# Performance work log

Hardware: AMD Instinct MI355X
Metric: run time of the kernel (lower is better)

The kernel has to match this reference:

```python
import jax, jax.numpy as jnp
import numpy as np

B = 8192          # tokens
D = 768           # activation_dim
N_EXP = 16        # experts
ED = 1536         # expert_dict_size = dict_size // experts
DICT = N_EXP * ED # 24576
K = 100           # sparse dict top-k
TOP_E = 2         # top-e expert selection


def setup_inputs() -> dict:
    key = jax.random.key(0)
    ks = jax.random.split(key, 5)
    x = jax.random.normal(ks[0], (B, D), dtype=jnp.float32)
    gate_W = jax.random.normal(ks[1], (N_EXP, D), dtype=jnp.float32) * 0.02
    gate_b = jnp.zeros((N_EXP,), jnp.float32)
    b_gate = jnp.zeros((D,), jnp.float32)
    b_dec = jnp.zeros((D,), jnp.float32)
    expert_W = jax.random.normal(ks[2], (N_EXP, ED, D), dtype=jnp.float32) * 0.02
    expert_b = jnp.zeros((N_EXP, ED), jnp.float32)
    dec = jax.random.normal(ks[3], (DICT, D), dtype=jnp.float32)
    decoder = dec / (jnp.linalg.norm(dec, axis=1, keepdims=True) + 1.1920929e-07)  # unit-norm rows
    return {"x": x, "gate_W": gate_W, "gate_b": gate_b, "b_gate": b_gate,
            "b_dec": b_dec, "expert_W": expert_W, "expert_b": expert_b,
            "decoder": decoder}


def reference(x, gate_W, gate_b, b_gate, b_dec, expert_W, expert_b, decoder):
    nb = x.shape[0]
    # --- gate: softmax over experts, keep top-e, renormalize (heaviside=False path)
    gate_logits = (x - b_gate) @ gate_W.T + gate_b            # [B, E]
    gate_scores = jax.nn.softmax(gate_logits, axis=-1)
    top_vals, top_idx = jax.lax.top_k(gate_scores, TOP_E)     # [B, e]
    # softmax over {-inf everywhere except top values} == softmax(top_vals) scattered
    renorm = jax.nn.softmax(top_vals, axis=-1)
    expert_mask = jnp.zeros_like(gate_scores).at[
        jnp.arange(nb)[:, None], top_idx].set(renorm)          # [B, E]
    # --- dense all-expert encode (faithful to source: computes every expert, then masks)
    z = jax.nn.relu(jnp.einsum('bd,ned->bne', x - b_dec, expert_W) + expert_b)  # [B, E, ED]
    f = (z * expert_mask[:, :, None]).reshape(nb, DICT)       # [B, dict_size]
    # --- top-k sparse dict decode (TritonDecoder equivalent)
    top_acts, top_indices = jax.lax.top_k(f, K)               # [B, k]
    x_hat = jnp.einsum('bk,bkd->bd', top_acts, decoder[top_indices]) + b_dec
    return x_hat
```

## Files before the change

kernel.cpp:

```cpp
#include <hip/hip_runtime.h>
#include <hip/hip_fp16.h>
#include <cstdint>
#include <cstddef>

#define NB    8192
#define DD    768
#define NE    16
#define NPAIR 256
#define EDD   1536
#define KTOP  100
#define MAXT  8192
#define CAND_MAX 256
#define K1BLK 2048
#define NSTEP 12
#define BKBYTES 128
#define CONF_ULP 6
#define BAND_ULP 5

typedef __attribute__((ext_vector_type(4))) float f32x4;
typedef __attribute__((ext_vector_type(8))) _Float16 f16x8;

#define VMCNT8() asm volatile("s_waitcnt vmcnt(8)" ::: "memory")
#define VMCNT4() asm volatile("s_waitcnt vmcnt(4)" ::: "memory")
#define VMCNT0() asm volatile("s_waitcnt vmcnt(0)" ::: "memory")

__device__ __forceinline__ unsigned short f2bf(float v) {
    unsigned int u = __float_as_uint(v);
    u += 0x7FFFu + ((u >> 16) & 1u);
    return (unsigned short)(u >> 16);
}
__device__ __forceinline__ float bf2f(unsigned short h) {
    return __uint_as_float(((unsigned int)h) << 16);
}
__device__ __forceinline__ unsigned short f2h_bits(float v) {
    return __half_as_ushort(__float2half(v));
}
__device__ __forceinline__ float h2f_bits(unsigned short b) {
    return __half2float(__ushort_as_half(b));
}
__device__ __forceinline__ void async16(const void* g, void* l) {
    __builtin_amdgcn_global_load_lds(
        (const __attribute__((address_space(1))) unsigned int*)g,
        (__attribute__((address_space(3))) unsigned int*)l, 16, 0, 0);
}

__global__ __launch_bounds__(256) void k0_cvt_bf(
    const float* __restrict__ src, unsigned short* __restrict__ dst)
{
    const int i = blockIdx.x * 256 + threadIdx.x;
    const float4 v = reinterpret_cast<const float4*>(src)[i];
    ushort4 h;
    h.x = f2bf(v.x); h.y = f2bf(v.y); h.z = f2bf(v.z); h.w = f2bf(v.w);
    reinterpret_cast<ushort4*>(dst)[i] = h;
}

__global__ __launch_bounds__(256) void k0_cvt_f16(
    const float* __restrict__ src, unsigned short* __restrict__ dst)
{
    const int i = blockIdx.x * 256 + threadIdx.x;
    const float4 v = reinterpret_cast<const float4*>(src)[i];
    ushort4 h;
    h.x = f2h_bits(v.x); h.y = f2h_bits(v.y); h.z = f2h_bits(v.z); h.w = f2h_bits(v.w);
    reinterpret_cast<ushort4*>(dst)[i] = h;
}

__global__ __launch_bounds__(256) void k1_gate(
    const float* __restrict__ x, const float* __restrict__ gate_W,
    const float* __restrict__ gate_b, const float* __restrict__ b_gate,
    const float* __restrict__ b_dec, unsigned short* __restrict__ xf16,
    int* __restrict__ eids, double* __restrict__ entw,
    int* __restrict__ rnk, int* __restrict__ blk_cnt,
    int* __restrict__ rnk0, unsigned char* __restrict__ blk_cntp)
{
    __shared__ int cnt[NE];
    __shared__ int cntp[NPAIR];
    const int wid  = threadIdx.x >> 6;
    const int lane = threadIdx.x & 63;
    const int blk  = blockIdx.x;
    const int tok  = blk * 4 + wid;

    if (threadIdx.x < NE) cnt[threadIdx.x] = 0;
    cntp[threadIdx.x] = 0;
    __syncthreads();

    double xv[12];
#pragma unroll
    for (int j = 0; j < 12; ++j) {
        const int k = j * 64 + lane;
        const float xr = x[(size_t)tok * DD + k];
        xv[j] = (double)xr - (double)b_gate[k];
        xf16[(size_t)tok * DD + k] = f2h_bits(xr - b_dec[k]);
    }

    double myLogit = -1.0e300;
    for (int e = 0; e < NE; ++e) {
        double d = 0.0;
#pragma unroll
        for (int j = 0; j < 12; ++j)
            d += xv[j] * (double)gate_W[e * DD + j * 64 + lane];
#pragma unroll
        for (int off = 32; off > 0; off >>= 1)
            d += __shfl_xor(d, off);
        if (lane == e) myLogit = d + (double)gate_b[e];
    }

    double m = myLogit;
#pragma unroll
    for (int off = 8; off > 0; off >>= 1) {
        double o = __shfl_xor(m, off); m = (o > m) ? o : m;
    }
    double p = exp(myLogit - m);
    double ssum = p;
#pragma unroll
    for (int off = 8; off > 0; off >>= 1) ssum += __shfl_xor(ssum, off);
    const double score = p / ssum;

    const bool lt16 = (lane < NE);
    double m1 = score;
#pragma unroll
    for (int off = 8; off > 0; off >>= 1) {
        double o = __shfl_xor(m1, off); m1 = (o > m1) ? o : m1;
    }
    unsigned long long b0 = __ballot(lt16 && (score == m1));
    const int i0 = __ffsll(b0) - 1;
    double sc2 = (lane == i0) ? -1.0 : score;
    double m2 = sc2;
#pragma unroll
    for (int off = 8; off > 0; off >>= 1) {
        double o = __shfl_xor(m2, off); m2 = (o > m2) ? o : m2;
    }
    unsigned long long b1 = __ballot(lt16 && (sc2 == m2));
    const int i1 = __ffsll(b1) - 1;

    if (lane == 0) {
        const double w0 = 1.0 / (1.0 + exp(m2 - m1));
        const double w1 = 1.0 - w0;
        eids[tok * 2 + 0] = i0;
        eids[tok * 2 + 1] = i1;
        entw[tok * 2 + 0] = w0;
        entw[tok * 2 + 1] = w1;
        rnk[tok * 2 + 0] = atomicAdd(&cnt[i0], 1);
        rnk[tok * 2 + 1] = atomicAdd(&cnt[i1], 1);
        rnk0[tok] = atomicAdd(&cntp[(i0 << 4) | i1], 1);
    }
    __syncthreads();
    if (threadIdx.x < NE)
        blk_cnt[threadIdx.x * K1BLK + blk] = cnt[threadIdx.x];
    blk_cntp[(size_t)threadIdx.x * K1BLK + blk] = (unsigned char)cntp[threadIdx.x];
}

__global__ __launch_bounds__(256) void k1_scan(
    const int* __restrict__ bc, int* __restrict__ bo, int* __restrict__ counts)
{
    __shared__ int tsum[256];
    const int e = blockIdx.x;
    const int t = threadIdx.x;
    int loc[8]; int s = 0;
#pragma unroll
    for (int i = 0; i < 8; ++i) { loc[i] = s; s += bc[e * K1BLK + t * 8 + i]; }
    tsum[t] = s;
    __syncthreads();
    for (int off = 1; off < 256; off <<= 1) {
        const int u = (t >= off) ? tsum[t - off] : 0;
        __syncthreads();
        tsum[t] += u;
        __syncthreads();
    }
    const int excl = tsum[t] - s;
#pragma unroll
    for (int i = 0; i < 8; ++i) bo[e * K1BLK + t * 8 + i] = excl + loc[i];
    if (t == 255) counts[e] = tsum[255];
}

__global__ __launch_bounds__(256) void k1_scanp(
    const unsigned char* __restrict__ bcp, unsigned short* __restrict__ bop,
    int* __restrict__ countsp)
{
    __shared__ int tsum[256];
    const int pp = blockIdx.x;
    const int t = threadIdx.x;
    int loc[8]; int s = 0;
#pragma unroll
    for (int i = 0; i < 8; ++i) { loc[i] = s; s += (int)bcp[(size_t)pp * K1BLK + t * 8 + i]; }
    tsum[t] = s;
    __syncthreads();
    for (int off = 1; off < 256; off <<= 1) {
        const int u = (t >= off) ? tsum[t - off] : 0;
        __syncthreads();
        tsum[t] += u;
        __syncthreads();
    }
    const int excl = tsum[t] - s;
#pragma unroll
    for (int i = 0; i < 8; ++i)
        bop[(size_t)pp * K1BLK + t * 8 + i] = (unsigned short)(excl + loc[i]);
    if (t == 255) countsp[pp] = tsum[255];
}

__global__ __launch_bounds__(256) void k1_base(
    const int* __restrict__ countsp, int* __restrict__ basep)
{
    __shared__ int ts[256];
    const int t = threadIdx.x;
    const int v = countsp[t];
    ts[t] = v;
    __syncthreads();
    for (int off = 1; off < 256; off <<= 1) {
        const int u = (t >= off) ? ts[t - off] : 0;
        __syncthreads();
        ts[t] += u;
        __syncthreads();
    }
    basep[t] = ts[t] - v;
}

__global__ __launch_bounds__(256) void k1_scatter(
    const int* __restrict__ eids, const int* __restrict__ rnk,
    const int* __restrict__ blk_off, int* __restrict__ lists,
    const int* __restrict__ rnk0, const unsigned short* __restrict__ bop,
    const int* __restrict__ basep, int* __restrict__ tokord)
{
    const int i = blockIdx.x * 256 + threadIdx.x;
    const int e = eids[i];
    const int blk = i >> 3;
    lists[e * MAXT + blk_off[e * K1BLK + blk] + rnk[i]] = i;
    if (!(i & 1)) {
        const int tok = i >> 1;
        const int pr = (e << 4) | eids[i | 1];
        tokord[basep[pr] + (int)bop[(size_t)pr * K1BLK + blk] + rnk0[tok]] = tok;
    }
}

template<bool WBF>
__global__ __launch_bounds__(256, 2) void k2_encode(
    const unsigned short* __restrict__ xf16,
    const unsigned short* __restrict__ wf16,
    const float* __restrict__ expert_W,
    const float* __restrict__ expert_b,
    const int* __restrict__ counts, const int* __restrict__ lists,
    const double* __restrict__ entw, unsigned short* __restrict__ fbuf)
{
    const int wg  = blockIdx.x;
    const int gw  = (wg & 7) * 1536 + (wg >> 3);
    const int e   = gw / 768;
    const int rem = gw % 768;
    const int cnt = counts[e];
    const int mbase = (rem / 12) * 128;
    if (mbase >= cnt) return;
    const int rows = min(128, cnt - mbase);
    const int nbase = (rem % 12) * 128;

    __shared__ char smem[65536];

    const int t = threadIdx.x;
    const int lane = t & 63;
    const int wid = t >> 6;
    const int wm = wid >> 1, wn = wid & 1;
    const int l15 = lane & 15, q = lane >> 4;
    const int rl = lane >> 3;
    const int cg = lane & 7;
    const int xorc = (cg ^ rl) << 4;

    size_t asrc[4];
#pragma unroll
    for (int j = 0; j < 4; ++j) {
        const int r = (wid * 4 + j) * 8 + rl;
        const int rr = (r < rows) ? r : 0;
        const int tok = lists[e * MAXT + mbase + rr] >> 1;
        asrc[j] = (size_t)tok * (DD * 2) + xorc;
    }
    size_t bsrc[4];
#pragma unroll
    for (int j = 0; j < 4; ++j) {
        const int r = (wid * 4 + j) * 8 + rl;
        bsrc[j] = ((size_t)(e * EDD + nbase + r)) * (DD * 2) + xorc;
    }
    const int kq = t & 15, rg = t >> 4;

    f32x4 acc[4][4];
#pragma unroll
    for (int a = 0; a < 4; ++a)
#pragma unroll
        for (int b = 0; b < 4; ++b)
            acc[a][b] = f32x4{0.f, 0.f, 0.f, 0.f};

    auto stageA = [&](int s, char* buf) {
#pragma unroll
        for (int j = 0; j < 4; ++j)
            async16((const char*)xf16 + asrc[j] + (size_t)s * BKBYTES,
                    buf + ((wid * 4 + j) << 10));
    };
    auto stageB_async = [&](int s, char* buf) {
#pragma unroll
        for (int j = 0; j < 4; ++j)
            async16((const char*)wf16 + bsrc[j] + (size_t)s * BKBYTES,
                    buf + 16384 + ((wid * 4 + j) << 10));
    };
    auto stageB_cvt = [&](int s, char* buf) {
#pragma unroll
        for (int j = 0; j < 8; ++j) {
            const int r = rg * 8 + j;
            const float4 bv = *reinterpret_cast<const float4*>(
                expert_W + ((size_t)e * EDD + nbase + r) * DD + s * 64 + kq * 4);
            ushort4 b4;
            b4.x = f2h_bits(bv.x); b4.y = f2h_bits(bv.y);
            b4.z = f2h_bits(bv.z); b4.w = f2h_bits(bv.w);
            *reinterpret_cast<ushort4*>(
                buf + 16384 + ((r * 128 + kq * 8) ^ ((r & 7) << 4))) = b4;
        }
    };
    auto compute = [&](char* buf) {
#pragma unroll
        for (int ks = 0; ks < 2; ++ks) {
            f16x8 ah[4], bh[4];
#pragma unroll
            for (int fm = 0; fm < 4; ++fm) {
                const int row = wm * 64 + fm * 16 + l15;
                ah[fm] = *reinterpret_cast<const f16x8*>(
                    buf + row * 128 + ((ks * 64 + q * 16) ^ ((row & 7) << 4)));
            }
#pragma unroll
            for (int fn = 0; fn < 4; ++fn) {
                const int row = wn * 64 + fn * 16 + l15;
                bh[fn] = *reinterpret_cast<const f16x8*>(
                    buf + 16384 + row * 128 + ((ks * 64 + q * 16) ^ ((row & 7) << 4)));
            }
#pragma unroll
            for (int fm = 0; fm < 4; ++fm)
#pragma unroll
                for (int fn = 0; fn < 4; ++fn)
                    acc[fm][fn] = __builtin_amdgcn_mfma_f32_16x16x32_f16(
                        ah[fm], bh[fn], acc[fm][fn], 0, 0, 0);
        }
    };

    if constexpr (WBF) {
        stageA(0, smem);
        stageB_async(0, smem);
    } else {
        stageB_cvt(0, smem);
        stageA(0, smem);
    }

    for (int s = 0; s < NSTEP; ++s) {
        char* cur = smem + ((s & 1) << 15);
        char* nxt = smem + (((s & 1) ^ 1) << 15);
        if (s + 1 < NSTEP) {
            if constexpr (WBF) {
                stageA(s + 1, nxt);
                stageB_async(s + 1, nxt);
                VMCNT8();
            } else {
                stageB_cvt(s + 1, nxt);
                stageA(s + 1, nxt);
                VMCNT4();
            }
        } else {
            VMCNT0();
        }
        __syncthreads();
        compute(cur);
        __syncthreads();
    }

#pragma unroll
    for (int fm = 0; fm < 4; ++fm) {
#pragma unroll
        for (int r = 0; r < 4; ++r) {
            const int ml = wm * 64 + fm * 16 + q * 4 + r;
            if (ml >= rows) continue;
            const int ent = lists[e * MAXT + mbase + ml];
            const float ren = (float)entw[ent];
            unsigned short* fout = fbuf + (size_t)ent * EDD + nbase;
#pragma unroll
            for (int fn = 0; fn < 4; ++fn) {
                const int nl = wn * 64 + fn * 16 + l15;
                float v = acc[fm][fn][r] + expert_b[e * EDD + nbase + nl];
                v = fmaxf(v, 0.f) * ren;
                fout[nl] = f2h_bits(v);
            }
        }
    }
}

template<int DEC16>
__global__ __launch_bounds__(256) void k3_topk_decode(
    const float* __restrict__ x, const float* __restrict__ b_dec,
    const float* __restrict__ expert_W, const float* __restrict__ expert_b,
    const int* __restrict__ eids, const double* __restrict__ entw,
    const unsigned short* __restrict__ fbuf,
    const float* __restrict__ decoder, const unsigned short* __restrict__ dec16,
    const int* __restrict__ tokord, float* __restrict__ out)
{
    const int bid = blockIdx.x;
    const int tok = tokord[(bid & 7) * (NB / 8) + (bid >> 3)];
    const int t = threadIdx.x;

    __shared__ __align__(16) char arena[12288];
    unsigned short* fv   = (unsigned short*)arena;
    unsigned int*   hist = (unsigned int*)(arena + 6144);
    int*            cidx = (int*)(arena + 7168);
    double*         cval = (double*)(arena + 8192);
    float*          red  = (float*)arena;
    __shared__ unsigned int sc[256];
    __shared__ int hb_s, T_s, rem_s, tz_s, nsel_s, ncand_s, total_s, need_s;
    __shared__ int   sel_didx[KTOP];
    __shared__ float sel_act[KTOP];

    const unsigned int* frow = reinterpret_cast<const unsigned int*>(fbuf + (size_t)tok * 2 * EDD);
#pragma unroll
    for (int i = 0; i < 6; ++i)
        reinterpret_cast<unsigned int*>(fv)[t + 256 * i] = frow[t + 256 * i];
    if (t == 0) { tz_s = 0; nsel_s = 0; ncand_s = 0; }
    hist[t] = 0u;
    __syncthreads();

#pragma unroll
    for (int i = 0; i < 12; ++i) {
        const unsigned int u = fv[t + 256 * i];
        if (u) atomicAdd(&hist[u >> 8], 1u);
    }
    __syncthreads();
    sc[t] = hist[t];
    __syncthreads();
    for (int off = 1; off < 256; off <<= 1) {
        const unsigned int v2 = (t < 256 - off) ? sc[t + off] : 0u;
        __syncthreads();
        sc[t] += v2;
        __syncthreads();
    }
    {
        const unsigned int above = (t == 255) ? 0u : sc[t + 1];
        if (sc[t] >= KTOP && above < KTOP) { hb_s = t; rem_s = KTOP - (int)above; }
        if (t == 0 && sc[0] < KTOP) tz_s = 1;
    }
    __syncthreads();

    if (!tz_s) {
        hist[t] = 0u;
        __syncthreads();
        const unsigned int hb = (unsigned int)hb_s;
#pragma unroll
        for (int i = 0; i < 12; ++i) {
            const unsigned int u = fv[t + 256 * i];
            if (u && (u >> 8) == hb) atomicAdd(&hist[u & 255u], 1u);
        }
        __syncthreads();
        sc[t] = hist[t];
        __syncthreads();
        for (int off = 1; off < 256; off <<= 1) {
            const unsigned int v2 = (t < 256 - off) ? sc[t + off] : 0u;
            __syncthreads();
            sc[t] += v2;
            __syncthreads();
        }
        {
            const unsigned int rem = (unsigned int)rem_s;
            const unsigned int above = (t == 255) ? 0u : sc[t + 1];
            if (sc[t] >= rem && above < rem) T_s = (hb_s << 8) | t;
        }
        __syncthreads();
    }

    if (tz_s) {
#pragma unroll
        for (int i = 0; i < 12; ++i) {
            const int j = t + 256 * i;
            const unsigned int u = fv[j];
            if (u) {
                const int p = atomicAdd(&nsel_s, 1);
                const int slot = (j >= EDD) ? 1 : 0;
                const int n = j - slot * EDD;
                sel_didx[p] = eids[tok * 2 + slot] * EDD + n;
                sel_act[p] = h2f_bits((unsigned short)u);
            }
        }
        __syncthreads();
        if (t == 0) total_s = nsel_s;
        __syncthreads();
    } else {
        const int T = T_s;
#pragma unroll
        for (int i = 0; i < 12; ++i) {
            const int j = t + 256 * i;
            const unsigned int u = fv[j];
            if ((int)u >= T + CONF_ULP) {
                const int p = atomicAdd(&nsel_s, 1);
                const int slot = (j >= EDD) ? 1 : 0;
                const int n = j - slot * EDD;
                sel_didx[p] = eids[tok * 2 + slot] * EDD + n;
                sel_act[p] = h2f_bits((unsigned short)u);
            } else if (u != 0u && (int)u + BAND_ULP >= T) {
                const int c = atomicAdd(&ncand_s, 1);
                if (c < CAND_MAX) cidx[c] = j;
            }
        }
        __syncthreads();

        {
            const int ncand = min(ncand_s, CAND_MAX);
            const int wv = t >> 6, lane = t & 63;
            for (int c = wv; c < ncand; c += 4) {
                const int j = cidx[c];
                const int slot = (j >= EDD) ? 1 : 0;
                const int n = j - slot * EDD;
                const int ee = eids[tok * 2 + slot];
                const float* wr = expert_W + ((size_t)ee * EDD + n) * DD;
                const float* xr = x + (size_t)tok * DD;
                double d = 0.0;
#pragma unroll
                for (int jj = 0; jj < 12; ++jj) {
                    const int k = jj * 64 + lane;
                    d += ((double)xr[k] - (double)b_dec[k]) * (double)wr[k];
                }
#pragma unroll
                for (int off = 32; off > 0; off >>= 1) d += __shfl_xor(d, off);
                if (lane == 0) {
                    double z = d + (double)expert_b[ee * EDD + n];
                    if (z < 0.0) z = 0.0;
                    cval[c] = z * entw[tok * 2 + slot];
                }
            }
        }
        __syncthreads();
        if (t == 0) {
            const int ncand = min(ncand_s, CAND_MAX);
            int need = KTOP - nsel_s;
            if (need > ncand) need = ncand;
            if (need < 0) need = 0;
            need_s = need;
            total_s = nsel_s + need;
        }
        __syncthreads();

        {
            const int ncand = min(ncand_s, CAND_MAX);
            if (t < ncand) {
                const int j = cidx[t];
                const int slot = (j >= EDD) ? 1 : 0;
                const int my_didx = eids[tok * 2 + slot] * EDD + (j - slot * EDD);
                const double v = cval[t];
                int rank = 0;
                for (int i = 0; i < ncand; ++i) {
                    const int ji = cidx[i];
                    const int si = (ji >= EDD) ? 1 : 0;
                    const int di = eids[tok * 2 + si] * EDD + (ji - si * EDD);
                    const double vi = cval[i];
                    rank += (vi > v) || (vi == v && di < my_didx);
                }
                if (rank < need_s) {
                    sel_didx[nsel_s + rank] = my_didx;
                    sel_act[nsel_s + rank] = (float)v;
                }
            }
        }
        __syncthreads();
    }

    const int total = total_s;
    const int wv = t >> 6;
    const int lane = t & 63;
    float accd[12];
#pragma unroll
    for (int i = 0; i < 12; ++i) accd[i] = 0.f;

    if (DEC16) {
        auto ldrow = [&](int k, float& a, ushort4& u0, ushort4& u1, ushort4& u2) {
            a = sel_act[k];
            const char* dr = (const char*)(dec16 + (size_t)sel_didx[k] * DD) + lane * 24;
            u0 = *reinterpret_cast<const ushort4*>(dr);
            u1 = *reinterpret_cast<const ushort4*>(dr + 8);
            u2 = *reinterpret_cast<const ushort4*>(dr + 16);
        };
        auto fmarow = [&](float a, ushort4 u0, ushort4 u1, ushort4 u2) {
            accd[0] += a * bf2f(u0.x);  accd[1]  += a * bf2f(u0.y);
            accd[2] += a * bf2f(u0.z);  accd[3]  += a * bf2f(u0.w);
            accd[4] += a * bf2f(u1.x);  accd[5]  += a * bf2f(u1.y);
            accd[6] += a * bf2f(u1.z);  accd[7]  += a * bf2f(u1.w);
            accd[8] += a * bf2f(u2.x);  accd[9]  += a * bf2f(u2.y);
            accd[10] += a * bf2f(u2.z); accd[11] += a * bf2f(u2.w);
        };
        int k = wv;
        for (; k + 12 < total; k += 16) {
            float a0, a1, a2, a3;
            ushort4 p00, p01, p02, p10, p11, p12, p20, p21, p22, p30, p31, p32;
            ldrow(k,      a0, p00, p01, p02);
            ldrow(k + 4,  a1, p10, p11, p12);
            ldrow(k + 8,  a2, p20, p21, p22);
            ldrow(k + 12, a3, p30, p31, p32);
            fmarow(a0, p00, p01, p02);
            fmarow(a1, p10, p11, p12);
            fmarow(a2, p20, p21, p22);
            fmarow(a3, p30, p31, p32);
        }
        for (; k < total; k += 4) {
            float a; ushort4 q0, q1, q2;
            ldrow(k, a, q0, q1, q2);
            fmarow(a, q0, q1, q2);
        }
    } else {
        auto body = [&](int k) {
            const float a = sel_act[k];
            const float* dr = decoder + (size_t)sel_didx[k] * DD + lane * 12;
            const float4 f0 = *reinterpret_cast<const float4*>(dr);
            const float4 f1 = *reinterpret_cast<const float4*>(dr + 4);
            const float4 f2 = *reinterpret_cast<const float4*>(dr + 8);
            accd[0] += a * f0.x;  accd[1]  += a * f0.y;
            accd[2] += a * f0.z;  accd[3]  += a * f0.w;
            accd[4] += a * f1.x;  accd[5]  += a * f1.y;
            accd[6] += a * f1.z;  accd[7]  += a * f1.w;
            accd[8] += a * f2.x;  accd[9]  += a * f2.y;
            accd[10] += a * f2.z; accd[11] += a * f2.w;
        };
        int k = wv;
        for (; k + 4 < total; k += 8) { body(k); body(k + 4); }
        if (k < total) body(k);
    }

#pragma unroll
    for (int i = 0; i < 12; ++i)
        red[wv * DD + lane * 12 + i] = accd[i];
    __syncthreads();
#pragma unroll
    for (int i = 0; i < 3; ++i) {
        const int j = t + 256 * i;
        out[(size_t)tok * DD + j] =
            red[j] + red[DD + j] + red[2 * DD + j] + red[3 * DD + j] + b_dec[j];
    }
}

__global__ void k_sentinel(float* __restrict__ out, int n) {
    int i = blockIdx.x * blockDim.x + threadIdx.x;
    if (i < n) out[i] = 12345.0f;
}

extern "C" void kernel_launch(void* const* d_in, const int* in_sizes, int n_in,
                              void* d_out, int out_size, void* d_ws, size_t ws_size,
                              hipStream_t stream)
{
    (void)in_sizes; (void)n_in;
    const float* x        = (const float*)d_in[0];
    const float* gate_W   = (const float*)d_in[1];
    const float* gate_b   = (const float*)d_in[2];
    const float* b_gate   = (const float*)d_in[3];
    const float* b_dec    = (const float*)d_in[4];
    const float* expert_W = (const float*)d_in[5];
    const float* expert_b = (const float*)d_in[6];
    const float* decoder  = (const float*)d_in[7];
    float* out = (float*)d_out;

    char* ws = (char*)d_ws;
    const size_t off_countsp = 1024;
    const size_t off_basep  = 2048;
    const size_t off_blkcnt = 4096;
    const size_t off_blkoff = off_blkcnt + (size_t)NE * K1BLK * 4;
    const size_t off_rnk    = off_blkoff + (size_t)NE * K1BLK * 4;
    const size_t off_eids   = off_rnk    + (size_t)NB * 2 * 4;
    const size_t off_entw   = off_eids   + (size_t)NB * 2 * 4;
    const size_t off_lists  = off_entw   + (size_t)NB * 2 * 8;
    const size_t off_fbuf   = off_lists  + (size_t)NE * MAXT * 4;
    const size_t off_xbf    = off_fbuf   + (size_t)NB * 2 * EDD * 2;
    const size_t off_bcp    = off_xbf    + (size_t)NB * DD * 2;
    const size_t off_bop    = off_bcp    + (size_t)NPAIR * K1BLK;
    const size_t off_rnk0   = off_bop    + (size_t)NPAIR * K1BLK * 2;
    const size_t off_tokord = off_rnk0   + (size_t)NB * 4;
    const size_t base_end   = off_tokord + (size_t)NB * 4;
    const size_t WSZ        = (size_t)NE * EDD * DD * 2;

    if (ws_size < base_end) {
        k_sentinel<<<(out_size + 255) / 256, 256, 0, stream>>>(out, out_size);
        return;
    }
    size_t off = base_end;
    const bool have_w = (ws_size >= off + WSZ);
    unsigned short* wf16 = have_w ? (unsigned short*)(ws + off) : nullptr;
    if (have_w) off += WSZ;
    const bool have_d = (ws_size >= off + WSZ);
    unsigned short* dec16v = have_d ? (unsigned short*)(ws + off) : nullptr;

    int*            counts  = (int*)ws;
    int*            countsp = (int*)(ws + off_countsp);
    int*            basep   = (int*)(ws + off_basep);
    int*            blk_cnt = (int*)(ws + off_blkcnt);
    int*            blk_off = (int*)(ws + off_blkoff);
    int*            rnk     = (int*)(ws + off_rnk);
    int*            eids    = (int*)(ws + off_eids);
    double*         entw    = (double*)(ws + off_entw);
    int*            lists   = (int*)(ws + off_lists);
    unsigned short* fbuf    = (unsigned short*)(ws + off_fbuf);
    unsigned short* xf16    = (unsigned short*)(ws + off_xbf);
    unsigned char*  blk_cntp= (unsigned char*)(ws + off_bcp);
    unsigned short* bop     = (unsigned short*)(ws + off_bop);
    int*            rnk0    = (int*)(ws + off_rnk0);
    int*            tokord  = (int*)(ws + off_tokord);

    const int n4blocks = (NE * EDD * DD / 4) / 256;
    if (have_w)
        k0_cvt_f16<<<n4blocks, 256, 0, stream>>>(expert_W, wf16);
    if (have_d)
        k0_cvt_bf<<<n4blocks, 256, 0, stream>>>(decoder, dec16v);

    k1_gate<<<K1BLK, 256, 0, stream>>>(x, gate_W, gate_b, b_gate, b_dec, xf16,
                                       eids, entw, rnk, blk_cnt, rnk0, blk_cntp);
    k1_scan<<<NE, 256, 0, stream>>>(blk_cnt, blk_off, counts);
    k1_scanp<<<NPAIR, 256, 0, stream>>>(blk_cntp, bop, countsp);
    k1_base<<<1, 256, 0, stream>>>(countsp, basep);
    k1_scatter<<<NB * 2 / 256, 256, 0, stream>>>(eids, rnk, blk_off, lists,
                                                 rnk0, bop, basep, tokord);

    if (have_w)
        k2_encode<true><<<12288, 256, 0, stream>>>(xf16, wf16, expert_W, expert_b,
                                                   counts, lists, entw, fbuf);
    else
        k2_encode<false><<<12288, 256, 0, stream>>>(xf16, wf16, expert_W, expert_b,
                                                    counts, lists, entw, fbuf);

    if (have_d)
        k3_topk_decode<1><<<NB, 256, 0, stream>>>(x, b_dec, expert_W, expert_b, eids,
                                                  entw, fbuf, decoder, dec16v, tokord, out);
    else
        k3_topk_decode<0><<<NB, 256, 0, stream>>>(x, b_dec, expert_W, expert_b, eids,
                                                  entw, fbuf, decoder, dec16v, tokord, out);
}
```

Before: 296.5 us.

## Compact expert encode grid with a device work list and fuse small launches

A single-block kernel now builds a compact list of (expert, row-tile) items from the per-expert counts. The encode kernel launches a fixed grid sized to the worst case (1728 blocks) instead of 12288, most of which used to exit immediately, and it keeps an XCD-aware swizzle over that list. The two weight-conversion kernels are merged into one launch, as are the two scan kernels, which cuts launch count. The cost is an extra indirection and device-side count reads at encode start, plus a serial loop in the base kernel.

```diff
diff --git a/kernel.cpp b/kernel.cpp
--- a/kernel.cpp
+++ b/kernel.cpp
@@ -16,6 +16,7 @@
 #define BKBYTES 128
 #define CONF_ULP 6
 #define BAND_ULP 5
+#define K2GRID 1728
 
 typedef __attribute__((ext_vector_type(4))) float f32x4;
 typedef __attribute__((ext_vector_type(8))) _Float16 f16x8;
@@ -62,6 +63,26 @@
     ushort4 h;
     h.x = f2h_bits(v.x); h.y = f2h_bits(v.y); h.z = f2h_bits(v.z); h.w = f2h_bits(v.w);
     reinterpret_cast<ushort4*>(dst)[i] = h;
+}
+
+__global__ __launch_bounds__(256) void k0_cvt_both(
+    const float* __restrict__ w, unsigned short* __restrict__ wf16,
+    const float* __restrict__ dec, unsigned short* __restrict__ d16, int half)
+{
+    const int b = blockIdx.x;
+    if (b < half) {
+        const int i = b * 256 + threadIdx.x;
+        const float4 v = reinterpret_cast<const float4*>(w)[i];
+        ushort4 h;
+        h.x = f2h_bits(v.x); h.y = f2h_bits(v.y); h.z = f2h_bits(v.z); h.w = f2h_bits(v.w);
+        reinterpret_cast<ushort4*>(wf16)[i] = h;
+    } else {
+        const int i = (b - half) * 256 + threadIdx.x;
+        const float4 v = reinterpret_cast<const float4*>(dec)[i];
+        ushort4 h;
+        h.x = f2bf(v.x); h.y = f2bf(v.y); h.z = f2bf(v.z); h.w = f2bf(v.w);
+        reinterpret_cast<ushort4*>(d16)[i] = h;
+    }
 }
 
 __global__ __launch_bounds__(256) void k1_gate(
@@ -149,61 +170,62 @@
     blk_cntp[(size_t)threadIdx.x * K1BLK + blk] = (unsigned char)cntp[threadIdx.x];
 }
 
-__global__ __launch_bounds__(256) void k1_scan(
-    const int* __restrict__ bc, int* __restrict__ bo, int* __restrict__ counts)
-{
-    __shared__ int tsum[256];
-    const int e = blockIdx.x;
-    const int t = threadIdx.x;
-    int loc[8]; int s = 0;
-#pragma unroll
-    for (int i = 0; i < 8; ++i) { loc[i] = s; s += bc[e * K1BLK + t * 8 + i]; }
-    tsum[t] = s;
-    __syncthreads();
-    for (int off = 1; off < 256; off <<= 1) {
-        const int u = (t >= off) ? tsum[t - off] : 0;
-        __syncthreads();
-        tsum[t] += u;
-        __syncthreads();
-    }
-    const int excl = tsum[t] - s;
-#pragma unroll
-    for (int i = 0; i < 8; ++i) bo[e * K1BLK + t * 8 + i] = excl + loc[i];
-    if (t == 255) counts[e] = tsum[255];
-}
-
-__global__ __launch_bounds__(256) void k1_scanp(
+__global__ __launch_bounds__(256) void k1_scans(
+    const int* __restrict__ bc, int* __restrict__ bo, int* __restrict__ counts,
     const unsigned char* __restrict__ bcp, unsigned short* __restrict__ bop,
     int* __restrict__ countsp)
 {
     __shared__ int tsum[256];
-    const int pp = blockIdx.x;
+    const int g = blockIdx.x;
     const int t = threadIdx.x;
-    int loc[8]; int s = 0;
-#pragma unroll
-    for (int i = 0; i < 8; ++i) { loc[i] = s; s += (int)bcp[(size_t)pp * K1BLK + t * 8 + i]; }
-    tsum[t] = s;
-    __syncthreads();
-    for (int off = 1; off < 256; off <<= 1) {
-        const int u = (t >= off) ? tsum[t - off] : 0;
-        __syncthreads();
-        tsum[t] += u;
-        __syncthreads();
-    }
-    const int excl = tsum[t] - s;
-#pragma unroll
-    for (int i = 0; i < 8; ++i)
-        bop[(size_t)pp * K1BLK + t * 8 + i] = (unsigned short)(excl + loc[i]);
-    if (t == 255) countsp[pp] = tsum[255];
-}
-
-__global__ __launch_bounds__(256) void k1_base(
-    const int* __restrict__ countsp, int* __restrict__ basep)
+    if (g < NE) {
+        const int e = g;
+        int loc[8]; int s = 0;
+#pragma unroll
+        for (int i = 0; i < 8; ++i) { loc[i] = s; s += bc[e * K1BLK + t * 8 + i]; }
+        tsum[t] = s;
+        __syncthreads();
+        for (int off = 1; off < 256; off <<= 1) {
+            const int u = (t >= off) ? tsum[t - off] : 0;
+            __syncthreads();
+            tsum[t] += u;
+            __syncthreads();
+        }
+        const int excl = tsum[t] - s;
+#pragma unroll
+        for (int i = 0; i < 8; ++i) bo[e * K1BLK + t * 8 + i] = excl + loc[i];
+        if (t == 255) counts[e] = tsum[255];
+    } else {
+        const int pp = g - NE;
+        int loc[8]; int s = 0;
+#pragma unroll
+        for (int i = 0; i < 8; ++i) { loc[i] = s; s += (int)bcp[(size_t)pp * K1BLK + t * 8 + i]; }
+        tsum[t] = s;
+        __syncthreads();
+        for (int off = 1; off < 256; off <<= 1) {
+            const int u = (t >= off) ? tsum[t - off] : 0;
+            __syncthreads();
+            tsum[t] += u;
+            __syncthreads();
+        }
+        const int excl = tsum[t] - s;
+#pragma unroll
+        for (int i = 0; i < 8; ++i)
+            bop[(size_t)pp * K1BLK + t * 8 + i] = (unsigned short)(excl + loc[i]);
+        if (t == 255) countsp[pp] = tsum[255];
+    }
+}
+
+__global__ __launch_bounds__(256) void k1_base_work(
+    const int* __restrict__ countsp, int* __restrict__ basep,
+    const int* __restrict__ counts, int* __restrict__ wl, int* __restrict__ nwk)
 {
     __shared__ int ts[256];
+    __shared__ int nm[NE], nb[NE + 1];
     const int t = threadIdx.x;
     const int v = countsp[t];
     ts[t] = v;
+    if (t < NE) nm[t] = (counts[t] + 127) >> 7;
     __syncthreads();
     for (int off = 1; off < 256; off <<= 1) {
         const int u = (t >= off) ? ts[t - off] : 0;
@@ -212,6 +234,15 @@
         __syncthreads();
     }
     basep[t] = ts[t] - v;
+    if (t == 0) {
+        int s = 0;
+        for (int e = 0; e < NE; ++e) { nb[e] = s; s += nm[e]; }
+        nb[NE] = s;
+        *nwk = s * 12;
+    }
+    __syncthreads();
+    if (t < NE)
+        for (int mt = 0; mt < nm[t]; ++mt) wl[nb[t] + mt] = (t << 8) | mt;
 }
 
 __global__ __launch_bounds__(256) void k1_scatter(
@@ -238,17 +269,22 @@
     const float* __restrict__ expert_W,
     const float* __restrict__ expert_b,
     const int* __restrict__ counts, const int* __restrict__ lists,
-    const double* __restrict__ entw, unsigned short* __restrict__ fbuf)
-{
-    const int wg  = blockIdx.x;
-    const int gw  = (wg & 7) * 1536 + (wg >> 3);
-    const int e   = gw / 768;
-    const int rem = gw % 768;
+    const double* __restrict__ entw, unsigned short* __restrict__ fbuf,
+    const int* __restrict__ wl, const int* __restrict__ nwk)
+{
+    const int bid = blockIdx.x;
+    const int nw = *nwk;
+    if (bid >= nw) return;
+    const int q = nw >> 3, r = nw & 7;
+    const int xcd = bid & 7, loc = bid >> 3;
+    const int swz = ((xcd < r) ? xcd * (q + 1) : r * (q + 1) + (xcd - r) * q) + loc;
+    const int item = wl[swz / 12];
+    const int e = item >> 8;
     const int cnt = counts[e];
-    const int mbase = (rem / 12) * 128;
+    const int mbase = (item & 255) * 128;
     if (mbase >= cnt) return;
     const int rows = min(128, cnt - mbase);
-    const int nbase = (rem % 12) * 128;
+    const int nbase = (swz % 12) * 128;
 
     __shared__ char smem[65536];
 
@@ -256,7 +292,7 @@
     const int lane = t & 63;
     const int wid = t >> 6;
     const int wm = wid >> 1, wn = wid & 1;
-    const int l15 = lane & 15, q = lane >> 4;
+    const int l15 = lane & 15, q4 = lane >> 4;
     const int rl = lane >> 3;
     const int cg = lane & 7;
     const int xorc = (cg ^ rl) << 4;
@@ -264,16 +300,16 @@
     size_t asrc[4];
 #pragma unroll
     for (int j = 0; j < 4; ++j) {
-        const int r = (wid * 4 + j) * 8 + rl;
-        const int rr = (r < rows) ? r : 0;
+        const int rr0 = (wid * 4 + j) * 8 + rl;
+        const int rr = (rr0 < rows) ? rr0 : 0;
         const int tok = lists[e * MAXT + mbase + rr] >> 1;
         asrc[j] = (size_t)tok * (DD * 2) + xorc;
     }
     size_t bsrc[4];
 #pragma unroll
     for (int j = 0; j < 4; ++j) {
-        const int r = (wid * 4 + j) * 8 + rl;
-        bsrc[j] = ((size_t)(e * EDD + nbase + r)) * (DD * 2) + xorc;
+        const int rr0 = (wid * 4 + j) * 8 + rl;
+        bsrc[j] = ((size_t)(e * EDD + nbase + rr0)) * (DD * 2) + xorc;
     }
     const int kq = t & 15, rg = t >> 4;
 
@@ -299,14 +335,14 @@
     auto stageB_cvt = [&](int s, char* buf) {
 #pragma unroll
         for (int j = 0; j < 8; ++j) {
-            const int r = rg * 8 + j;
+            const int rr0 = rg * 8 + j;
             const float4 bv = *reinterpret_cast<const float4*>(
-                expert_W + ((size_t)e * EDD + nbase + r) * DD + s * 64 + kq * 4);
+                expert_W + ((size_t)e * EDD + nbase + rr0) * DD + s * 64 + kq * 4);
             ushort4 b4;
             b4.x = f2h_bits(bv.x); b4.y = f2h_bits(bv.y);
             b4.z = f2h_bits(bv.z); b4.w = f2h_bits(bv.w);
             *reinterpret_cast<ushort4*>(
-                buf + 16384 + ((r * 128 + kq * 8) ^ ((r & 7) << 4))) = b4;
+                buf + 16384 + ((rr0 * 128 + kq * 8) ^ ((rr0 & 7) << 4))) = b4;
         }
     };
     auto compute = [&](char* buf) {
@@ -317,13 +353,13 @@
             for (int fm = 0; fm < 4; ++fm) {
                 const int row = wm * 64 + fm * 16 + l15;
                 ah[fm] = *reinterpret_cast<const f16x8*>(
-                    buf + row * 128 + ((ks * 64 + q * 16) ^ ((row & 7) << 4)));
+                    buf + row * 128 + ((ks * 64 + q4 * 16) ^ ((row & 7) << 4)));
             }
 #pragma unroll
             for (int fn = 0; fn < 4; ++fn) {
                 const int row = wn * 64 + fn * 16 + l15;
                 bh[fn] = *reinterpret_cast<const f16x8*>(
-                    buf + 16384 + row * 128 + ((ks * 64 + q * 16) ^ ((row & 7) << 4)));
+                    buf + 16384 + row * 128 + ((ks * 64 + q4 * 16) ^ ((row & 7) << 4)));
             }
 #pragma unroll
             for (int fm = 0; fm < 4; ++fm)
@@ -367,7 +403,7 @@
     for (int fm = 0; fm < 4; ++fm) {
 #pragma unroll
         for (int r = 0; r < 4; ++r) {
-            const int ml = wm * 64 + fm * 16 + q * 4 + r;
+            const int ml = wm * 64 + fm * 16 + q4 * 4 + r;
             if (ml >= rows) continue;
             const int ent = lists[e * MAXT + mbase + ml];
             const float ren = (float)entw[ent];
@@ -664,7 +700,9 @@
     const size_t off_bop    = off_bcp    + (size_t)NPAIR * K1BLK;
     const size_t off_rnk0   = off_bop    + (size_t)NPAIR * K1BLK * 2;
     const size_t off_tokord = off_rnk0   + (size_t)NB * 4;
-    const size_t base_end   = off_tokord + (size_t)NB * 4;
+    const size_t off_wl     = off_tokord + (size_t)NB * 4;
+    const size_t off_nwk    = off_wl     + 4096;
+    const size_t base_end   = off_nwk    + 64;
     const size_t WSZ        = (size_t)NE * EDD * DD * 2;
 
     if (ws_size < base_end) {
@@ -693,27 +731,32 @@
     unsigned short* bop     = (unsigned short*)(ws + off_bop);
     int*            rnk0    = (int*)(ws + off_rnk0);
     int*            tokord  = (int*)(ws + off_tokord);
+    int*            wl      = (int*)(ws + off_wl);
+    int*            nwk     = (int*)(ws + off_nwk);
 
     const int n4blocks = (NE * EDD * DD / 4) / 256;
-    if (have_w)
+    if (have_w && have_d)
+        k0_cvt_both<<<2 * n4blocks, 256, 0, stream>>>(expert_W, wf16, decoder,
+                                                      dec16v, n4blocks);
+    else if (have_w)
         k0_cvt_f16<<<n4blocks, 256, 0, stream>>>(expert_W, wf16);
-    if (have_d)
+    else if (have_d)
         k0_cvt_bf<<<n4blocks, 256, 0, stream>>>(decoder, dec16v);
 
     k1_gate<<<K1BLK, 256, 0, stream>>>(x, gate_W, gate_b, b_gate, b_dec, xf16,
                                        eids, entw, rnk, blk_cnt, rnk0, blk_cntp);
-    k1_scan<<<NE, 256, 0, stream>>>(blk_cnt, blk_off, counts);
-    k1_scanp<<<NPAIR, 256, 0, stream>>>(blk_cntp, bop, countsp);
-    k1_base<<<1, 256, 0, stream>>>(countsp, basep);
+    k1_scans<<<NE + NPAIR, 256, 0, stream>>>(blk_cnt, blk_off, counts,
+                                             blk_cntp, bop, countsp);
+    k1_base_work<<<1, 256, 0, stream>>>(countsp, basep, counts, wl, nwk);
     k1_scatter<<<NB * 2 / 256, 256, 0, stream>>>(eids, rnk, blk_off, lists,
                                                  rnk0, bop, basep, tokord);
 
     if (have_w)
-        k2_encode<true><<<12288, 256, 0, stream>>>(xf16, wf16, expert_W, expert_b,
-                                                   counts, lists, entw, fbuf);
+        k2_encode<true><<<K2GRID, 256, 0, stream>>>(xf16, wf16, expert_W, expert_b,
+                                                    counts, lists, entw, fbuf, wl, nwk);
     else
-        k2_encode<false><<<12288, 256, 0, stream>>>(xf16, wf16, expert_W, expert_b,
-                                                    counts, lists, entw, fbuf);
+        k2_encode<false><<<K2GRID, 256, 0, stream>>>(xf16, wf16, expert_W, expert_b,
+                                                     counts, lists, entw, fbuf, wl, nwk);
 
     if (have_d)
         k3_topk_decode<1><<<NB, 256, 0, stream>>>(x, b_dec, expert_W, expert_b, eids,
```

After: 302.0 us. Within noise of the previous version (+1.9%).
